# Kernel tuning notes

Measured on AMD Instinct MI355X. Metric: run time of the kernel, lower is better.

Reference implementation:

```python
import jax, jax.numpy as jnp
import numpy as np

N = 100000      # nodes
E = 3200000     # edges (avg degree 32, undirected)
FIN = 256
FOUT = 256
K = 4


def setup_inputs() -> dict:
    key = jax.random.key(0)
    k1, k2, k3 = jax.random.split(key, 3)
    x = jax.random.normal(k1, (N, FIN), dtype=jnp.float32)
    edge_index = jax.random.randint(k2, (2, E), 0, N, dtype=jnp.int32)
    stdv = 1.0 / np.sqrt(FIN * K)
    # K per-hop dense projection weights, uniform(-stdv, stdv) as in reset_parameters
    weights = jax.random.uniform(k3, (K, FIN, FOUT), dtype=jnp.float32,
                                 minval=-stdv, maxval=stdv)
    return {"x": x, "edge_index": edge_index, "weights": weights}


def reference(x, edge_index, weights):
    # edge_index -> symmetric adjacency S (from_edgelist builds an undirected graph):
    # spmm(S, z)[i] = sum over neighbors j of z[j]; scatter-add both directions.
    src, dst = edge_index[0], edge_index[1]

    def spmm(z):
        out = jnp.zeros_like(z).at[dst].add(z[src])
        return out.at[src].add(z[dst])

    zs = [x]
    for _ in range(1, weights.shape[0]):
        x = spmm(x)           # [N, Fin] k-hop diffused features
        zs.append(x)
    # sum_k zs[k] @ weights[k]  -> [N, Fout]
    return jnp.einsum('knf,kfo->no', jnp.stack(zs), weights)
```

## Files before the change

kernel.cpp:

```cpp
#include <hip/hip_runtime.h>
#include <hip/hip_bf16.h>


#define NNODES 100000
#define NEDGES 3200000
#define FOUTF  256
#define MPAD   100096
#define MTILES 782
#define NB     782
#define FILLB  1024
#define CHUNK  3125

typedef __attribute__((ext_vector_type(4))) int   i32x4;
typedef __attribute__((ext_vector_type(4))) float f32x4;

__device__ __forceinline__ void async_ld16(const void* g, void* l) {
  __builtin_amdgcn_global_load_lds(
      (const __attribute__((address_space(1))) unsigned int*)g,
      (__attribute__((address_space(3))) unsigned int*)l, 16, 0, 0);
}


__global__ __launch_bounds__(256)
void bucket_count_kernel(const int* __restrict__ ei, int* __restrict__ bcount) {
  __shared__ int h[NB];
  for (int i = threadIdx.x; i < NB; i += 256) h[i] = 0;
  __syncthreads();
  for (int e = blockIdx.x * 256 + threadIdx.x; e < NEDGES; e += gridDim.x * 256) {
    int s = ei[e];
    int d = ei[NEDGES + e];
    atomicAdd(&h[d >> 7], 1);
    atomicAdd(&h[s >> 7], 1);
  }
  __syncthreads();
  for (int i = threadIdx.x; i < NB; i += 256) {
    int c = h[i];
    if (c) atomicAdd(&bcount[i], c);
  }
}

__global__ __launch_bounds__(1024)
void bucket_scan_kernel(const int* __restrict__ bcount, int* __restrict__ bbase,
                        int* __restrict__ bcursor) {
  __shared__ int ws[16];
  int t = threadIdx.x, lane = t & 63, wv = t >> 6;
  int v = (t < NB) ? bcount[t] : 0;
  int s = v;
  #pragma unroll
  for (int off = 1; off < 64; off <<= 1) {
    int tmp = __shfl_up(s, off, 64);
    if (lane >= off) s += tmp;
  }
  if (lane == 63) ws[wv] = s;
  __syncthreads();
  if (t == 0) {
    int run = 0;
    #pragma unroll
    for (int k = 0; k < 16; ++k) { int tmp = ws[k]; ws[k] = run; run += tmp; }
  }
  __syncthreads();
  int excl = s + ws[wv] - v;
  if (t < NB) { bbase[t] = excl; bcursor[t] = excl; }
  if (t == NB) bbase[NB] = excl;
}

__global__ __launch_bounds__(256)
void bin_fill_kernel(const int* __restrict__ ei, int* __restrict__ bcursor,
                     unsigned int* __restrict__ binned) {
  __shared__ int h[NB];
  for (int i = threadIdx.x; i < NB; i += 256) h[i] = 0;
  __syncthreads();
  const int e0 = blockIdx.x * CHUNK;
  const int e1 = (e0 + CHUNK < NEDGES) ? e0 + CHUNK : NEDGES;
  for (int e = e0 + threadIdx.x; e < e1; e += 256) {
    int s = ei[e];
    int d = ei[NEDGES + e];
    atomicAdd(&h[d >> 7], 1);
    atomicAdd(&h[s >> 7], 1);
  }
  __syncthreads();
  for (int i = threadIdx.x; i < NB; i += 256) {
    int c = h[i];
    h[i] = c ? atomicAdd(&bcursor[i], c) : 0;
  }
  __syncthreads();
  for (int e = e0 + threadIdx.x; e < e1; e += 256) {
    int s = ei[e];
    int d = ei[NEDGES + e];
    int p = atomicAdd(&h[d >> 7], 1);
    binned[p] = ((unsigned int)(d & 127) << 17) | (unsigned int)s;
    int q = atomicAdd(&h[s >> 7], 1);
    binned[q] = ((unsigned int)(s & 127) << 17) | (unsigned int)d;
  }
}

__global__ __launch_bounds__(256)
void bucket_csr_kernel(const unsigned int* __restrict__ binned,
                       const int* __restrict__ bbase,
                       int* __restrict__ row_ptr, int* __restrict__ adj) {
  __shared__ int cnt[128];
  __shared__ int cur[128];
  const int b = blockIdx.x;
  const int node0 = b << 7;
  const int base = bbase[b];
  const int end = bbase[b + 1];
  const int tid = threadIdx.x;
  if (tid < 128) cnt[tid] = 0;
  __syncthreads();
  for (int i = base + tid; i < end; i += 256) {
    unsigned int v = binned[i];
    atomicAdd(&cnt[v >> 17], 1);
  }
  __syncthreads();
  if (tid < 128) {
    int ex = 0;
    #pragma unroll 8
    for (int j = 0; j < 128; ++j) {
      int c = cnt[j];
      ex += (j < tid) ? c : 0;
    }
    int node = node0 + tid;
    if (node < NNODES) row_ptr[node] = base + ex;
    cur[tid] = base + ex;
  }
  if (tid == 0 && b == NB - 1) row_ptr[NNODES] = end;
  __syncthreads();
  for (int i = base + tid; i < end; i += 256) {
    unsigned int v = binned[i];
    int nbr = (int)(v & 0x1FFFFu);
    int p = atomicAdd(&cur[v >> 17], 1);
    adj[p] = nbr << 8;
  }
}


__global__ __launch_bounds__(256)
void convert_x_kernel(const float* __restrict__ x,
                      unsigned char* __restrict__ g0,
                      float* __restrict__ sc0) {
  const int row = (blockIdx.x * 256 + threadIdx.x) >> 6;
  const int lane = threadIdx.x & 63;
  if (row >= NNODES) return;
  float4 xv = *(const float4*)&x[(size_t)row * 256 + (lane << 2)];

  float m = fmaxf(fmaxf(fabsf(xv.x), fabsf(xv.y)), fmaxf(fabsf(xv.z), fabsf(xv.w)));
  #pragma unroll
  for (int i = 1; i < 64; i <<= 1) m = fmaxf(m, __shfl_xor(m, i, 64));
  float inv = (m > 0.f) ? 127.f / m : 0.f;
  int q0 = (int)__builtin_rintf(xv.x * inv);
  int q1 = (int)__builtin_rintf(xv.y * inv);
  int q2 = (int)__builtin_rintf(xv.z * inv);
  int q3 = (int)__builtin_rintf(xv.w * inv);
  *(unsigned int*)(g0 + (size_t)row * 256 + (lane << 2)) =
      ((unsigned)q0 & 255u) | (((unsigned)q1 & 255u) << 8) |
      (((unsigned)q2 & 255u) << 16) | (((unsigned)q3 & 255u) << 24);
  if (lane == 0) sc0[row] = m * (1.f / 127.f);
}

__global__ __launch_bounds__(256)
void wmax_kernel(const float* __restrict__ w, unsigned int* __restrict__ dWmax) {
  __shared__ float red[4];
  const int k = blockIdx.x >> 6;
  const int chunk = blockIdx.x & 63;
  const float* wk = w + (size_t)k * 65536 + chunk * 1024;
  float m = 0.f;
  #pragma unroll
  for (int i = 0; i < 4; ++i) m = fmaxf(m, fabsf(wk[threadIdx.x + i * 256]));
  #pragma unroll
  for (int i = 1; i < 64; i <<= 1) m = fmaxf(m, __shfl_xor(m, i, 64));
  if ((threadIdx.x & 63) == 0) red[threadIdx.x >> 6] = m;
  __syncthreads();
  if (threadIdx.x == 0) {
    m = fmaxf(fmaxf(red[0], red[1]), fmaxf(red[2], red[3]));
    atomicMax(&dWmax[k], __float_as_uint(m));
  }
}

__global__ void quantw_kernel(const float* __restrict__ w,
                              const unsigned int* __restrict__ dWmax,
                              signed char* __restrict__ W8) {
  int idx = blockIdx.x * 256 + threadIdx.x;
  int k = idx >> 16, f = (idx >> 8) & 255, o = idx & 255;
  float mx = __uint_as_float(dWmax[k]);
  float inv = (mx > 0.f) ? 127.f / mx : 0.f;
  W8[(size_t)k * 65536 + o * 256 + f] = (signed char)(int)__builtin_rintf(w[idx] * inv);
}


#define DECQ(vv, ss)                                        \
  { acc0 += (ss) * (float)((vv) & 255u);                    \
    acc1 += (ss) * (float)(((vv) >> 8) & 255u);             \
    acc2 += (ss) * (float)(((vv) >> 16) & 255u);            \
    acc3 += (ss) * (float)((vv) >> 24);                     \
    ssum += (ss); }

__global__ __launch_bounds__(256)
void spmm_q8_kernel(const unsigned char* __restrict__ gin,
                    const float* __restrict__ sin,
                    unsigned char* __restrict__ gout,
                    float* __restrict__ sout,
                    const int* __restrict__ row_ptr,
                    const int* __restrict__ adjb) {
  const int wid = __builtin_amdgcn_readfirstlane((blockIdx.x * 256 + threadIdx.x) >> 6);
  const int lane = threadIdx.x & 63;
  if (wid >= NNODES) return;
  const int beg = row_ptr[wid];
  const int end = row_ptr[wid + 1];
  const int lb = lane << 2;
  const char* scb = (const char*)sin;

  float acc0 = 0.f, acc1 = 0.f, acc2 = 0.f, acc3 = 0.f, ssum = 0.f;
  int j = beg;
  for (; j + 4 <= end; j += 4) {
    int o0 = adjb[j + 0], o1 = adjb[j + 1], o2 = adjb[j + 2], o3 = adjb[j + 3];
    float s0 = *(const float*)(scb + (o0 >> 6));
    float s1 = *(const float*)(scb + (o1 >> 6));
    float s2 = *(const float*)(scb + (o2 >> 6));
    float s3 = *(const float*)(scb + (o3 >> 6));
    unsigned int v0 = *(const unsigned int*)(gin + o0 + lb) ^ 0x80808080u;
    unsigned int v1 = *(const unsigned int*)(gin + o1 + lb) ^ 0x80808080u;
    unsigned int v2 = *(const unsigned int*)(gin + o2 + lb) ^ 0x80808080u;
    unsigned int v3 = *(const unsigned int*)(gin + o3 + lb) ^ 0x80808080u;
    DECQ(v0, s0); DECQ(v1, s1); DECQ(v2, s2); DECQ(v3, s3);
  }
  for (; j < end; ++j) {
    int o = adjb[j];
    float s = *(const float*)(scb + (o >> 6));
    unsigned int v = *(const unsigned int*)(gin + o + lb) ^ 0x80808080u;
    DECQ(v, s);
  }

  const float bias = 128.f * ssum;
  const float a0 = acc0 - bias;
  const float a1 = acc1 - bias;
  const float a2 = acc2 - bias;
  const float a3 = acc3 - bias;

  float m = fmaxf(fmaxf(fabsf(a0), fabsf(a1)), fmaxf(fabsf(a2), fabsf(a3)));
  #pragma unroll
  for (int i = 1; i < 64; i <<= 1) m = fmaxf(m, __shfl_xor(m, i, 64));
  float inv = (m > 0.f) ? 127.f / m : 0.f;
  int q0 = (int)__builtin_rintf(a0 * inv);
  int q1 = (int)__builtin_rintf(a1 * inv);
  int q2 = (int)__builtin_rintf(a2 * inv);
  int q3 = (int)__builtin_rintf(a3 * inv);
  *(unsigned int*)(gout + (size_t)wid * 256 + lb) =
      ((unsigned)q0 & 255u) | (((unsigned)q1 & 255u) << 8) |
      (((unsigned)q2 & 255u) << 16) | (((unsigned)q3 & 255u) << 24);
  if (lane == 0) sout[wid] = m * (1.f / 127.f);
}


__global__ __launch_bounds__(512)
void gemm_i8_kernel(const unsigned char* __restrict__ q0p,
                    const unsigned char* __restrict__ q1p,
                    const unsigned char* __restrict__ q2p,
                    const unsigned char* __restrict__ q3p,
                    const float* __restrict__ s0p,
                    const float* __restrict__ s1p,
                    const float* __restrict__ s2p,
                    const float* __restrict__ s3p,
                    const signed char* __restrict__ W8,
                    const unsigned int* __restrict__ dWmax,
                    float* __restrict__ C) {
  __shared__ __align__(16) unsigned char As[128 * 128];
  __shared__ __align__(16) unsigned char Bs[256 * 128];
  const int tid = threadIdx.x;
  const int lane = tid & 63;
  const int wave = tid >> 6;
  const int wr = wave >> 2;
  const int wc = wave & 3;
  const int rowA_base = blockIdx.x * 128;

  const unsigned char* qs[4] = {q0p, q1p, q2p, q3p};
  const float* scs[4] = {s0p, s1p, s2p, s3p};

  f32x4 accf[4][4] = {};

  #pragma unroll
  for (int k = 0; k < 4; ++k) {
    const unsigned char* Qk = qs[k];
    const signed char* Wk = W8 + (size_t)k * 65536;
    i32x4 acci[4][4] = {};
    #pragma unroll
    for (int kc = 0; kc < 2; ++kc) {
      __syncthreads();
      #pragma unroll
      for (int i = 0; i < 2; ++i) {
        int slot = tid + 512 * i;
        int row = slot >> 3;
        int col = ((slot & 7) << 4) ^ ((row & 7) << 4);
        async_ld16(Qk + (size_t)(rowA_base + row) * 256 + kc * 128 + col,
                   &As[slot * 16]);
      }
      #pragma unroll
      for (int i = 0; i < 4; ++i) {
        int slot = tid + 512 * i;
        int row = slot >> 3;
        int col = ((slot & 7) << 4) ^ ((row & 7) << 4);
        async_ld16(Wk + (size_t)row * 256 + kc * 128 + col, &Bs[slot * 16]);
      }
      __syncthreads();
      #pragma unroll
      for (int kk = 0; kk < 2; ++kk) {
        const int kb = kk * 64 + ((lane >> 4) << 4);
        i32x4 a[4], b[4];
        #pragma unroll
        for (int m = 0; m < 4; ++m) {
          int row = wr * 64 + m * 16 + (lane & 15);
          a[m] = *(const i32x4*)&As[row * 128 + (kb ^ ((row & 7) << 4))];
        }
        #pragma unroll
        for (int n = 0; n < 4; ++n) {
          int row = wc * 64 + n * 16 + (lane & 15);
          b[n] = *(const i32x4*)&Bs[row * 128 + (kb ^ ((row & 7) << 4))];
        }
        #pragma unroll
        for (int m = 0; m < 4; ++m) {
          #pragma unroll
          for (int n = 0; n < 4; ++n)
            acci[m][n] = __builtin_amdgcn_mfma_i32_16x16x64_i8(a[m], b[n], acci[m][n], 0, 0, 0);
        }
      }
    }
    const float dWk = __uint_as_float(dWmax[k]) * (1.f / 127.f);
    const float* sk = scs[k];
    #pragma unroll
    for (int m = 0; m < 4; ++m) {
      #pragma unroll
      for (int j = 0; j < 4; ++j) {
        int r = rowA_base + wr * 64 + ((lane >> 4) << 2) + m * 16 + j;
        float s = sk[r] * dWk;
        #pragma unroll
        for (int n = 0; n < 4; ++n)
          accf[m][n][j] += s * (float)acci[m][n][j];
      }
    }
  }

  const int ccol0 = wc * 64 + (lane & 15);
  const int crow0 = rowA_base + wr * 64 + ((lane >> 4) << 2);
  #pragma unroll
  for (int m = 0; m < 4; ++m) {
    #pragma unroll
    for (int j = 0; j < 4; ++j) {
      int r = crow0 + m * 16 + j;
      if (r < NNODES) {
        float* cp = C + (size_t)r * FOUTF + ccol0;
        #pragma unroll
        for (int n = 0; n < 4; ++n) cp[n * 16] = accf[m][n][j];
      }
    }
  }
}


extern "C" void kernel_launch(void* const* d_in, const int* in_sizes, int n_in,
                              void* d_out, int out_size, void* d_ws, size_t ws_size,
                              hipStream_t stream) {
  (void)in_sizes; (void)n_in; (void)out_size; (void)ws_size;
  const float* x  = (const float*)d_in[0];
  const int*   ei = (const int*)d_in[1];
  const float* w  = (const float*)d_in[2];
  float* out = (float*)d_out;

  char* ws = (char*)d_ws;
  size_t off = 0;
  auto carve = [&](size_t bytes) -> void* {
    void* p = ws + off;
    off = (off + bytes + 255) & ~(size_t)255;
    return p;
  };
  unsigned char* gA = (unsigned char*)carve((size_t)MPAD * 256);
  unsigned char* gB = (unsigned char*)carve((size_t)MPAD * 256);
  unsigned char* gC = (unsigned char*)carve((size_t)MPAD * 256);
  unsigned char* gD = (unsigned char*)carve((size_t)MPAD * 256);
  float* scA        = (float*)carve((size_t)MPAD * 4);
  float* scB        = (float*)carve((size_t)MPAD * 4);
  float* scC        = (float*)carve((size_t)MPAD * 4);
  float* scD        = (float*)carve((size_t)MPAD * 4);
  signed char* W8   = (signed char*)carve((size_t)4 * 65536);
  unsigned int* dWmax = (unsigned int*)carve(4 * 4);
  int* row_ptr      = (int*)carve((size_t)(NNODES + 1) * 4);
  int* adj          = (int*)carve((size_t)2 * NEDGES * 4);
  int* bcount       = (int*)carve((size_t)(NB + 1) * 4);
  int* bbase        = (int*)carve((size_t)(NB + 1) * 4);
  int* bcursor      = (int*)carve((size_t)(NB + 1) * 4);
  unsigned int* binned = (unsigned int*)gD;

  hipMemsetAsync(bcount, 0, (size_t)(NB + 1) * 4, stream);
  hipMemsetAsync(dWmax, 0, 16, stream);

  bucket_count_kernel<<<1024, 256, 0, stream>>>(ei, bcount);
  bucket_scan_kernel<<<1, 1024, 0, stream>>>(bcount, bbase, bcursor);
  bin_fill_kernel<<<FILLB, 256, 0, stream>>>(ei, bcursor, binned);
  bucket_csr_kernel<<<NB, 256, 0, stream>>>(binned, bbase, row_ptr, adj);

  convert_x_kernel<<<25000, 256, 0, stream>>>(x, gA, scA);
  wmax_kernel<<<256, 256, 0, stream>>>(w, dWmax);
  quantw_kernel<<<1024, 256, 0, stream>>>(w, dWmax, W8);

  spmm_q8_kernel<<<25000, 256, 0, stream>>>(gA, scA, gB, scB, row_ptr, adj);
  spmm_q8_kernel<<<25000, 256, 0, stream>>>(gB, scB, gC, scC, row_ptr, adj);
  spmm_q8_kernel<<<25000, 256, 0, stream>>>(gC, scC, gD, scD, row_ptr, adj);

  gemm_i8_kernel<<<MTILES, 512, 0, stream>>>(gA, gB, gC, gD, scA, scB, scC, scD,
                                             W8, dWmax, out);
}
```

Baseline: 1.028 ms.

## Replace atomic bucket cursors with per-chunk count table and two-level scan

```diff
diff --git a/kernel.cpp b/kernel.cpp
--- a/kernel.cpp
+++ b/kernel.cpp
@@ -8,7 +8,7 @@
 #define MPAD   100096
 #define MTILES 782
 #define NB     782
-#define FILLB  1024
+#define NCHUNK 1024
 #define CHUNK  3125
 
 typedef __attribute__((ext_vector_type(4))) int   i32x4;
@@ -22,51 +22,7 @@
 
 
 __global__ __launch_bounds__(256)
-void bucket_count_kernel(const int* __restrict__ ei, int* __restrict__ bcount) {
-  __shared__ int h[NB];
-  for (int i = threadIdx.x; i < NB; i += 256) h[i] = 0;
-  __syncthreads();
-  for (int e = blockIdx.x * 256 + threadIdx.x; e < NEDGES; e += gridDim.x * 256) {
-    int s = ei[e];
-    int d = ei[NEDGES + e];
-    atomicAdd(&h[d >> 7], 1);
-    atomicAdd(&h[s >> 7], 1);
-  }
-  __syncthreads();
-  for (int i = threadIdx.x; i < NB; i += 256) {
-    int c = h[i];
-    if (c) atomicAdd(&bcount[i], c);
-  }
-}
-
-__global__ __launch_bounds__(1024)
-void bucket_scan_kernel(const int* __restrict__ bcount, int* __restrict__ bbase,
-                        int* __restrict__ bcursor) {
-  __shared__ int ws[16];
-  int t = threadIdx.x, lane = t & 63, wv = t >> 6;
-  int v = (t < NB) ? bcount[t] : 0;
-  int s = v;
-  #pragma unroll
-  for (int off = 1; off < 64; off <<= 1) {
-    int tmp = __shfl_up(s, off, 64);
-    if (lane >= off) s += tmp;
-  }
-  if (lane == 63) ws[wv] = s;
-  __syncthreads();
-  if (t == 0) {
-    int run = 0;
-    #pragma unroll
-    for (int k = 0; k < 16; ++k) { int tmp = ws[k]; ws[k] = run; run += tmp; }
-  }
-  __syncthreads();
-  int excl = s + ws[wv] - v;
-  if (t < NB) { bbase[t] = excl; bcursor[t] = excl; }
-  if (t == NB) bbase[NB] = excl;
-}
-
-__global__ __launch_bounds__(256)
-void bin_fill_kernel(const int* __restrict__ ei, int* __restrict__ bcursor,
-                     unsigned int* __restrict__ binned) {
+void chunk_count_kernel(const int* __restrict__ ei, int* __restrict__ cntg) {
   __shared__ int h[NB];
   for (int i = threadIdx.x; i < NB; i += 256) h[i] = 0;
   __syncthreads();
@@ -79,17 +35,76 @@
     atomicAdd(&h[s >> 7], 1);
   }
   __syncthreads();
-  for (int i = threadIdx.x; i < NB; i += 256) {
-    int c = h[i];
-    h[i] = c ? atomicAdd(&bcursor[i], c) : 0;
-  }
-  __syncthreads();
+  for (int i = threadIdx.x; i < NB; i += 256)
+    cntg[blockIdx.x * NB + i] = h[i];
+}
+
+__global__ __launch_bounds__(256)
+void scan_chunks_kernel(int* __restrict__ cntg, int* __restrict__ tot) {
+  __shared__ int ws2[4];
+  const int v = blockIdx.x;
+  const int t = threadIdx.x, lane = t & 63, wv = t >> 6;
+  int c[4];
+  int sum = 0;
+  #pragma unroll
+  for (int i = 0; i < 4; ++i) { c[i] = cntg[(4 * t + i) * NB + v]; sum += c[i]; }
+  int s = sum;
+  #pragma unroll
+  for (int off = 1; off < 64; off <<= 1) {
+    int tmp = __shfl_up(s, off, 64);
+    if (lane >= off) s += tmp;
+  }
+  if (lane == 63) ws2[wv] = s;
+  __syncthreads();
+  int wpre = 0;
+  #pragma unroll
+  for (int k = 0; k < 4; ++k) wpre += (k < wv) ? ws2[k] : 0;
+  int run = wpre + s - sum;
+  #pragma unroll
+  for (int i = 0; i < 4; ++i) { int tmp = c[i]; cntg[(4 * t + i) * NB + v] = run; run += tmp; }
+  if (t == 255) tot[v] = wpre + s;
+}
+
+__global__ __launch_bounds__(1024)
+void base_scan_kernel(const int* __restrict__ tot, int* __restrict__ bbase) {
+  __shared__ int ws[16];
+  int t = threadIdx.x, lane = t & 63, wv = t >> 6;
+  int v = (t < NB) ? tot[t] : 0;
+  int s = v;
+  #pragma unroll
+  for (int off = 1; off < 64; off <<= 1) {
+    int tmp = __shfl_up(s, off, 64);
+    if (lane >= off) s += tmp;
+  }
+  if (lane == 63) ws[wv] = s;
+  __syncthreads();
+  if (t == 0) {
+    int run = 0;
+    #pragma unroll
+    for (int k = 0; k < 16; ++k) { int tmp = ws[k]; ws[k] = run; run += tmp; }
+  }
+  __syncthreads();
+  int excl = s + ws[wv] - v;
+  if (t < NB) bbase[t] = excl;
+  if (t == NB) bbase[NB] = excl;
+}
+
+__global__ __launch_bounds__(256)
+void fill_kernel(const int* __restrict__ ei, const int* __restrict__ cntg,
+                 const int* __restrict__ bbase, unsigned int* __restrict__ binned) {
+  __shared__ int cur[NB];
+  const int b = blockIdx.x;
+  for (int i = threadIdx.x; i < NB; i += 256)
+    cur[i] = bbase[i] + cntg[b * NB + i];
+  __syncthreads();
+  const int e0 = b * CHUNK;
+  const int e1 = (e0 + CHUNK < NEDGES) ? e0 + CHUNK : NEDGES;
   for (int e = e0 + threadIdx.x; e < e1; e += 256) {
     int s = ei[e];
     int d = ei[NEDGES + e];
-    int p = atomicAdd(&h[d >> 7], 1);
+    int p = atomicAdd(&cur[d >> 7], 1);
     binned[p] = ((unsigned int)(d & 127) << 17) | (unsigned int)s;
-    int q = atomicAdd(&h[s >> 7], 1);
+    int q = atomicAdd(&cur[s >> 7], 1);
     binned[q] = ((unsigned int)(s & 127) << 17) | (unsigned int)d;
   }
 }
@@ -383,17 +398,17 @@
   unsigned int* dWmax = (unsigned int*)carve(4 * 4);
   int* row_ptr      = (int*)carve((size_t)(NNODES + 1) * 4);
   int* adj          = (int*)carve((size_t)2 * NEDGES * 4);
-  int* bcount       = (int*)carve((size_t)(NB + 1) * 4);
+  int* cntg         = (int*)carve((size_t)NCHUNK * NB * 4);
+  int* tot          = (int*)carve((size_t)NB * 4);
   int* bbase        = (int*)carve((size_t)(NB + 1) * 4);
-  int* bcursor      = (int*)carve((size_t)(NB + 1) * 4);
   unsigned int* binned = (unsigned int*)gD;
 
-  hipMemsetAsync(bcount, 0, (size_t)(NB + 1) * 4, stream);
   hipMemsetAsync(dWmax, 0, 16, stream);
 
-  bucket_count_kernel<<<1024, 256, 0, stream>>>(ei, bcount);
-  bucket_scan_kernel<<<1, 1024, 0, stream>>>(bcount, bbase, bcursor);
-  bin_fill_kernel<<<FILLB, 256, 0, stream>>>(ei, bcursor, binned);
+  chunk_count_kernel<<<NCHUNK, 256, 0, stream>>>(ei, cntg);
+  scan_chunks_kernel<<<NB, 256, 0, stream>>>(cntg, tot);
+  base_scan_kernel<<<1, 1024, 0, stream>>>(tot, bbase);
+  fill_kernel<<<NCHUNK, 256, 0, stream>>>(ei, cntg, bbase, binned);
   bucket_csr_kernel<<<NB, 256, 0, stream>>>(binned, bbase, row_ptr, adj);
 
   convert_x_kernel<<<25000, 256, 0, stream>>>(x, gA, scA);
```

New measurement: 1.002 ms. 1.03x faster.
